# Performance work log

Measured on AMD Instinct MI355X. Metric: run time of the kernel, lower is better.

The kernel has to match this reference:

```python
import jax, jax.numpy as jnp
import numpy as np

NUM_GROUPS = 32
EPS = 1e-6


def group_norm(x, gamma, beta):
    # x: (B, C, H, W)
    B, C, H, W = x.shape
    g = x.reshape(B, NUM_GROUPS, C // NUM_GROUPS, H, W)
    mean = g.mean(axis=(2, 3, 4), keepdims=True)
    var = g.var(axis=(2, 3, 4), keepdims=True)
    g = (g - mean) / jnp.sqrt(var + EPS)
    g = g.reshape(B, C, H, W)
    return g * gamma[None, :, None, None] + beta[None, :, None, None]


def nin(x, W, b):
    # 1x1 linear projection over channel dim
    return jnp.einsum('bchw,cd->bdhw', x, W) + b[None, :, None, None]


def setup_inputs() -> dict:
    key = jax.random.key(0)
    ks = jax.random.split(key, 8)
    B, C, H, W = 32, 512, 32, 32
    lim = np.sqrt(3 * 0.1 / C)  # NIN init_scale=0.1 uniform limit
    return {
        'x': jax.random.normal(ks[0], (B, C, H, W), jnp.float32),
        'gamma': jnp.ones((C,), jnp.float32),
        'beta': jnp.zeros((C,), jnp.float32),
        'Wq': jax.random.uniform(ks[1], (C, C), jnp.float32, -lim, lim),
        'bq': jnp.zeros((C,), jnp.float32),
        'Wk': jax.random.uniform(ks[2], (C, C), jnp.float32, -lim, lim),
        'bk': jnp.zeros((C,), jnp.float32),
        'Wv': jax.random.uniform(ks[3], (C, C), jnp.float32, -lim, lim),
        'bv': jnp.zeros((C,), jnp.float32),
        'Wp': jax.random.normal(ks[4], (C, C), jnp.float32) * 1e-5,  # init_scale=0.0 -> ~0
        'bp': jnp.zeros((C,), jnp.float32),
    }


def reference(x, gamma, beta, Wq, bq, Wk, bk, Wv, bv, Wp, bp):
    B, C, H, W = x.shape
    h = group_norm(x, gamma, beta)
    q = nin(h, Wq, bq)
    k = nin(h, Wk, bk)
    v = nin(h, Wv, bv)
    # full (HW)x(HW) attention weights, as the original materializes
    w = jnp.einsum('bchw,bcHW->bhwHW', q, k) * (C ** -0.5)
    w = w.reshape(B, H, W, H * W)
    w = jax.nn.softmax(w, axis=-1)
    w = w.reshape(B, H, W, H, W)
    h_out = jnp.einsum('bhwHW,bcHW->bchw', w, v)
    h_out = nin(h_out, Wp, bp)
    return x + h_out
```

## Files before the change

kernel.cpp:

```cpp
#include <hip/hip_runtime.h>
#include <hip/hip_bf16.h>
#include <math.h>

typedef __attribute__((ext_vector_type(8))) short bf16x8;
typedef __attribute__((ext_vector_type(4))) float f32x4;

typedef const __attribute__((address_space(1))) unsigned int guint;
typedef __attribute__((address_space(3))) unsigned int luint;

static __device__ __forceinline__ short f2bf(float f) {
    union { float f; unsigned u; } a; a.f = f;
    unsigned r = 0x7FFFu + ((a.u >> 16) & 1u);
    return (short)((a.u + r) >> 16);
}
static __device__ __forceinline__ float bf2f(short s) {
    union { unsigned u; float f; } a;
    a.u = ((unsigned)(unsigned short)s) << 16;
    return a.f;
}

__global__ __launch_bounds__(256)
void cast_w3(const float* __restrict__ wq, const float* __restrict__ wk,
             const float* __restrict__ wv, short* __restrict__ out)
{
    const float* W = (blockIdx.y == 0) ? wq : (blockIdx.y == 1) ? wk : wv;
    short* O = out + (long long)blockIdx.y * 262144;
    int i = (blockIdx.x * 256 + threadIdx.x) * 8;
    float4 a = *reinterpret_cast<const float4*>(W + i);
    float4 b = *reinterpret_cast<const float4*>(W + i + 4);
    bf16x8 o;
    o[0] = f2bf(a.x); o[1] = f2bf(a.y); o[2] = f2bf(a.z); o[3] = f2bf(a.w);
    o[4] = f2bf(b.x); o[5] = f2bf(b.y); o[6] = f2bf(b.z); o[7] = f2bf(b.w);
    *reinterpret_cast<bf16x8*>(O + i) = o;
}

__global__ __launch_bounds__(256)
void transpose_w(const float* __restrict__ w0, const float* __restrict__ w1,
                 const float* __restrict__ w2, const float* __restrict__ w3,
                 short* __restrict__ outT, float qscale)
{
    __shared__ float ld[32][33];
    const float* W = (blockIdx.z == 0) ? w0 : (blockIdx.z == 1) ? w1
                   : (blockIdx.z == 2) ? w2 : w3;
    const float sc = (blockIdx.z == 0) ? qscale : 1.f;
    short* O = outT + (long long)blockIdx.z * 512 * 512;
    const int tx = threadIdx.x & 31, ty = threadIdx.x >> 5;
    const int c0 = blockIdx.y * 32, d0 = blockIdx.x * 32;
#pragma unroll
    for (int r = 0; r < 4; ++r)
        ld[ty + 8 * r][tx] = W[(long long)(c0 + ty + 8 * r) * 512 + d0 + tx];
    __syncthreads();
#pragma unroll
    for (int r = 0; r < 4; ++r)
        O[(long long)(d0 + ty + 8 * r) * 512 + c0 + tx] = f2bf(ld[tx][ty + 8 * r] * sc);
}

__global__ __launch_bounds__(256)
void vec_pre2(const float* __restrict__ Wp, const float* __restrict__ bp,
              const float* __restrict__ bv, const float* __restrict__ Wk,
              const float* __restrict__ bq, float* __restrict__ b2,
              float* __restrict__ wkbq)
{
    __shared__ float red[256];
    const int t = threadIdx.x;
    const int o = blockIdx.x * 32 + (t >> 3);
    const int part = t & 7;
    float a = 0.f;
    if (blockIdx.y == 0) {
        for (int d = part * 64; d < part * 64 + 64; ++d)
            a += bv[d] * Wp[d * 512 + o];
    } else {
        for (int d = part * 64; d < part * 64 + 64; ++d)
            a += Wk[o * 512 + d] * bq[d];
    }
    red[t] = a; __syncthreads();
    if (part < 4) red[t] += red[t + 4];
    __syncthreads();
    if (part < 2) red[t] += red[t + 2];
    __syncthreads();
    if (part == 0) {
        float v = red[t] + red[t + 1];
        if (blockIdx.y == 0) b2[o] = v + bp[o];
        else wkbq[o] = v;
    }
}

__global__ __launch_bounds__(256)
void small_nt(const short* __restrict__ A, const short* __restrict__ B,
              short* __restrict__ C, float scale, int K,
              int lda, int ldb, int ldc, int tilesM)
{
    __shared__ short lsA[128 * 64];
    __shared__ short lsB[128 * 64];
    const int m0 = (blockIdx.x % tilesM) * 128;
    const int n0 = (blockIdx.x / tilesM) * 128;
    const int t = threadIdx.x;
    const int lane = t & 63;
    const int w = t >> 6;
    const int wr = w >> 1, wc = w & 1;
    const int lr16 = lane & 15, lkg = lane >> 4;
    const int srow = 32 * w + (lane >> 3);
    const int scol = (lane & 7) * 8;
    const short* gA = A + (long long)(m0 + srow) * lda + scol;
    const short* gB = B + (long long)(n0 + srow) * ldb + scol;

    f32x4 acc[4][4];
#pragma unroll
    for (int i = 0; i < 4; ++i)
#pragma unroll
        for (int j = 0; j < 4; ++j) acc[i][j] = (f32x4){0.f, 0.f, 0.f, 0.f};

    const int nk = K >> 6;
    for (int kt = 0; kt < nk; ++kt) {
        const short* ga = gA + kt * 64;
        const short* gb = gB + kt * 64;
#pragma unroll
        for (int c = 0; c < 4; ++c) {
            __builtin_amdgcn_global_load_lds(
                (guint*)(ga + (long long)(8 * c) * lda),
                (luint*)&lsA[(32 * w + 8 * c) * 64], 16, 0, 0);
            __builtin_amdgcn_global_load_lds(
                (guint*)(gb + (long long)(8 * c) * ldb),
                (luint*)&lsB[(32 * w + 8 * c) * 64], 16, 0, 0);
        }
        __syncthreads();
#pragma unroll
        for (int ks = 0; ks < 2; ++ks) {
            bf16x8 af[4], bfr[4];
#pragma unroll
            for (int mi = 0; mi < 4; ++mi)
                af[mi] = *reinterpret_cast<const bf16x8*>(
                    &lsA[(wr * 64 + mi * 16 + lr16) * 64 + ks * 32 + lkg * 8]);
#pragma unroll
            for (int ni = 0; ni < 4; ++ni)
                bfr[ni] = *reinterpret_cast<const bf16x8*>(
                    &lsB[(wc * 64 + ni * 16 + lr16) * 64 + ks * 32 + lkg * 8]);
#pragma unroll
            for (int mi = 0; mi < 4; ++mi)
#pragma unroll
                for (int ni = 0; ni < 4; ++ni)
                    acc[mi][ni] = __builtin_amdgcn_mfma_f32_16x16x32_bf16(
                        af[mi], bfr[ni], acc[mi][ni], 0, 0, 0);
        }
        __syncthreads();
    }
#pragma unroll
    for (int mi = 0; mi < 4; ++mi)
#pragma unroll
        for (int ni = 0; ni < 4; ++ni) {
            const int col = n0 + wc * 64 + ni * 16 + lr16;
#pragma unroll
            for (int j = 0; j < 4; ++j) {
                const int rrow = m0 + wr * 64 + mi * 16 + lkg * 4 + j;
                C[(long long)rrow * ldc + col] = f2bf(acc[mi][ni][j] * scale);
            }
        }
}

__global__ __launch_bounds__(256)
void gn_fused(const float* __restrict__ x, const float* __restrict__ gamma,
              const float* __restrict__ beta, short* __restrict__ hn,
              short* __restrict__ hnT)
{
    __shared__ float xs[16 * 1024];
    __shared__ float red[256];
    const int bg = blockIdx.x;
    const int g  = bg & 31, b = bg >> 5;
    const int t  = threadIdx.x;
    const float4* px = reinterpret_cast<const float4*>(x + (long long)bg * 16384);
    float s = 0.f, ss = 0.f;
#pragma unroll
    for (int i = 0; i < 16; ++i) {
        float4 v = px[t + 256 * i];
        reinterpret_cast<float4*>(xs)[t + 256 * i] = v;
        s  += v.x + v.y + v.z + v.w;
        ss += v.x * v.x + v.y * v.y + v.z * v.z + v.w * v.w;
    }
    red[t] = s; __syncthreads();
    for (int o = 128; o > 0; o >>= 1) {
        if (t < o) red[t] += red[t + o];
        __syncthreads();
    }
    const float mean = red[0] * (1.f / 16384.f);
    __syncthreads();
    red[t] = ss; __syncthreads();
    for (int o = 128; o > 0; o >>= 1) {
        if (t < o) red[t] += red[t + o];
        __syncthreads();
    }
    const float var  = red[0] * (1.f / 16384.f) - mean * mean;
    const float rstd = rsqrtf(var + 1e-6f);

    const int half = t & 1;
    float ga[8], be[8];
#pragma unroll
    for (int cc = 0; cc < 8; ++cc) {
        ga[cc] = gamma[g * 16 + half * 8 + cc];
        be[cc] = beta[g * 16 + half * 8 + cc];
    }
    short* outB = hn + (long long)bg * 16384;
#pragma unroll
    for (int it = 0; it < 8; ++it) {
        const int sidx = it * 128 + (t >> 1);
        bf16x8 o;
#pragma unroll
        for (int cc = 0; cc < 8; ++cc) {
            float v = xs[(half * 8 + cc) * 1024 + sidx];
            o[cc] = f2bf((v - mean) * rstd * ga[cc] + be[cc]);
        }
        *reinterpret_cast<bf16x8*>(outB + sidx * 16 + half * 8) = o;
    }
    short* oT = hnT + ((long long)b * 512 + g * 16) * 1024;
#pragma unroll
    for (int cc = 0; cc < 16; ++cc) {
        const float g_ = gamma[g * 16 + cc], b_ = beta[g * 16 + cc];
        const int pos = t * 4;
        short4 o4;
        o4.x = f2bf((xs[cc * 1024 + pos + 0] - mean) * rstd * g_ + b_);
        o4.y = f2bf((xs[cc * 1024 + pos + 1] - mean) * rstd * g_ + b_);
        o4.z = f2bf((xs[cc * 1024 + pos + 2] - mean) * rstd * g_ + b_);
        o4.w = f2bf((xs[cc * 1024 + pos + 3] - mean) * rstd * g_ + b_);
        *reinterpret_cast<short4*>(oT + cc * 1024 + pos) = o4;
    }
}

__global__ __launch_bounds__(256)
void colv_k(const short* __restrict__ hnT, const float* __restrict__ wkbq,
            float* __restrict__ colv, float qs)
{
    const int b = blockIdx.y, j = blockIdx.x * 256 + threadIdx.x;
    const short* p = hnT + (long long)b * 512 * 1024 + j;
    float a = 0.f;
    for (int c = 0; c < 512; ++c) a += wkbq[c] * bf2f(p[c * 1024]);
    colv[b * 1024 + j] = a * qs;
}

template<int BIAS_M, int BIAS_NB, int RESID, int EXPRS, int DIVROW4, int HN_A, int HN_B>
__global__ __launch_bounds__(512, 1)
void nt_gemm(const short* __restrict__ A, const short* __restrict__ B,
             void* __restrict__ Cv,
             const float* __restrict__ biasM, const float* __restrict__ biasN,
             const float* __restrict__ resid, float* __restrict__ rs,
             float scale, int K, int lda, int ldb, int ldc,
             long long sA, long long sB, long long sC,
             int tilesM, int tilesPerBatch)
{
    __shared__ short lsA[2][2][128 * 64];
    __shared__ short lsB[2][2][128 * 64];

    const int id = blockIdx.x;
    const int chunk = gridDim.x >> 3;
    const int gid = chunk ? ((id & 7) * chunk + (id >> 3)) : id;
    const int bz = gid / tilesPerBatch;
    const int tt = gid - bz * tilesPerBatch;
    const int m0 = (tt % tilesM) * 256;
    const int n0 = (tt / tilesM) * 256;

    const int t = threadIdx.x;
    const int lane = t & 63;
    const int w = t >> 6;
    const int wrs = w >> 1;
    const int wcs = w & 1;
    const int lr16 = lane & 15, lkg = lane >> 4;
    const int sw = lr16 & 7;

    const int srow = t >> 3;
    const int jch  = (t & 7) ^ (srow & 7);
    const int scol = jch * 8;

    const short* gA; int rsA, ktA;
    if (HN_A) {
        gA = A + ((long long)bz * 32 + (jch >> 1)) * 16384
               + (long long)(m0 + srow) * 16 + (jch & 1) * 8;
        rsA = 16; ktA = 65536;
    } else {
        gA = A + (long long)bz * sA + (long long)(m0 + srow) * lda + scol;
        rsA = lda; ktA = 64;
    }
    const short* gB; int rsB, ktB;
    if (HN_B) {
        gB = B + ((long long)bz * 32 + (jch >> 1)) * 16384
               + (long long)(n0 + srow) * 16 + (jch & 1) * 8;
        rsB = 16; ktB = 65536;
    } else {
        gB = B + (long long)bz * sB + (long long)(n0 + srow) * ldb + scol;
        rsB = ldb; ktB = 64;
    }

    f32x4 acc[4][2][4];
#pragma unroll
    for (int q = 0; q < 4; ++q)
#pragma unroll
        for (int i = 0; i < 2; ++i)
#pragma unroll
            for (int j = 0; j < 4; ++j) acc[q][i][j] = (f32x4){0.f, 0.f, 0.f, 0.f};

    const int nk = K >> 6;

#define STAGE_A(buf, h, kt)                                                    \
    {                                                                          \
        _Pragma("unroll")                                                      \
        for (int c = 0; c < 2; ++c)                                            \
            __builtin_amdgcn_global_load_lds(                                  \
                (guint*)(gA + (long long)(kt) * ktA                            \
                            + (long long)((h) * 128 + 64 * c) * rsA),          \
                (luint*)&lsA[buf][h][t * 8 + 4096 * c], 16, 0, 0);             \
    }
#define STAGE_B(buf, h, kt)                                                    \
    {                                                                          \
        _Pragma("unroll")                                                      \
        for (int c = 0; c < 2; ++c)                                            \
            __builtin_amdgcn_global_load_lds(                                  \
                (guint*)(gB + (long long)(kt) * ktB                            \
                            + (long long)((h) * 128 + 64 * c) * rsB),          \
                (luint*)&lsB[buf][h][t * 8 + 4096 * c], 16, 0, 0);             \
    }

#define LDA_HALF(dst, buf, h)                                                  \
    _Pragma("unroll")                                                          \
    for (int mi2 = 0; mi2 < 2; ++mi2)                                          \
        _Pragma("unroll")                                                      \
        for (int ks = 0; ks < 2; ++ks)                                         \
            dst[mi2][ks] = *reinterpret_cast<const bf16x8*>(                   \
                &lsA[buf][h][(wrs * 32 + mi2 * 16 + lr16) * 64 +               \
                             (((ks * 4 + lkg) ^ sw) * 8)]);
#define LDB_HALF(dst, buf, h)                                                  \
    _Pragma("unroll")                                                          \
    for (int ni = 0; ni < 4; ++ni)                                             \
        _Pragma("unroll")                                                      \
        for (int ks = 0; ks < 2; ++ks)                                         \
            dst[ni][ks] = *reinterpret_cast<const bf16x8*>(                    \
                &lsB[buf][h][(wcs * 64 + ni * 16 + lr16) * 64 +                \
                             (((ks * 4 + lkg) ^ sw) * 8)]);

#define MFMAQ(q, Af, Bf)                                                       \
    _Pragma("unroll")                                                          \
    for (int ks = 0; ks < 2; ++ks)                                             \
        _Pragma("unroll")                                                      \
        for (int mi2 = 0; mi2 < 2; ++mi2)                                      \
            _Pragma("unroll")                                                  \
            for (int ni = 0; ni < 4; ++ni)                                     \
                acc[q][mi2][ni] = __builtin_amdgcn_mfma_f32_16x16x32_bf16(     \
                    Af[mi2][ks], Bf[ni][ks], acc[q][mi2][ni], 0, 0, 0);

#define PH_END(N)                                                              \
    asm volatile("s_waitcnt vmcnt(" #N ")" ::: "memory");                      \
    __builtin_amdgcn_s_barrier();                                              \
    __builtin_amdgcn_sched_barrier(0)

#define FRAME(b, kt)                                                           \
    {                                                                          \
        bf16x8 a0[2][2], a1[2][2], b0f[4][2], b1f[4][2];                       \
        LDB_HALF(b0f, b, 0)                                                    \
        LDA_HALF(a0, b, 0)                                                     \
        LDB_HALF(b1f, b, 1)                                                    \
        STAGE_B((b) ^ 1, 0, (kt) + 1);                                         \
        STAGE_B((b) ^ 1, 1, (kt) + 1);                                         \
        STAGE_A((b) ^ 1, 0, (kt) + 1);                                         \
        MFMAQ(0, a0, b0f)                                                      \
        MFMAQ(1, a0, b1f)                                                      \
        PH_END(6);                                                             \
        LDA_HALF(a1, b, 1)                                                     \
        STAGE_A((b) ^ 1, 1, (kt) + 1);                                         \
        MFMAQ(2, a1, b0f)                                                      \
        MFMAQ(3, a1, b1f)                                                      \
        PH_END(2);                                                             \
    }

    STAGE_B(0, 0, 0); STAGE_B(0, 1, 0); STAGE_A(0, 0, 0);
    STAGE_A(0, 1, 0);
    PH_END(2);

    for (int kt = 0; kt < nk; kt += 2) {
        FRAME(0, kt)
        FRAME(1, kt + 1)
    }
#undef STAGE_A
#undef STAGE_B
#undef LDA_HALF
#undef LDB_HALF
#undef MFMAQ
#undef PH_END
#undef FRAME

    float psum[2][2][4];
    if (EXPRS) {
#pragma unroll
        for (int ah = 0; ah < 2; ++ah)
#pragma unroll
            for (int mi2 = 0; mi2 < 2; ++mi2)
#pragma unroll
                for (int j = 0; j < 4; ++j) psum[ah][mi2][j] = 0.f;
    }
#pragma unroll
    for (int ah = 0; ah < 2; ++ah) {
#pragma unroll
        for (int bh = 0; bh < 2; ++bh) {
#pragma unroll
            for (int mi2 = 0; mi2 < 2; ++mi2) {
                float addm[4], mul[4];
#pragma unroll
                for (int j = 0; j < 4; ++j) {
                    const int rrow = m0 + ah * 128 + wrs * 32 + mi2 * 16 + lkg * 4 + j;
                    addm[j] = BIAS_M ? biasM[rrow] : 0.f;
                    if (DIVROW4) {
                        const float* r4 = rs + (long long)bz * 4096 + rrow;
                        mul[j] = 1.f / (r4[0] + r4[1024] + r4[2048] + r4[3072]);
                    } else mul[j] = 1.f;
                }
#pragma unroll
                for (int ni = 0; ni < 4; ++ni) {
                    const int col = n0 + bh * 128 + wcs * 64 + ni * 16 + lr16;
                    float bn = BIAS_NB ? biasN[(long long)bz * 1024 + col] : 0.f;
#pragma unroll
                    for (int j = 0; j < 4; ++j) {
                        const int rrow = m0 + ah * 128 + wrs * 32 + mi2 * 16 + lkg * 4 + j;
                        float v2 = acc[ah * 2 + bh][mi2][ni][j] + addm[j] + bn;
                        v2 *= scale;
                        if (EXPRS) { v2 = __expf(v2 - 8.f); psum[ah][mi2][j] += v2; }
                        if (DIVROW4) v2 *= mul[j];
                        const long long idx = (long long)rrow * ldc + col;
                        if (RESID) {
                            float* Cf = (float*)Cv + (long long)bz * sC;
                            Cf[idx] = v2 + resid[(long long)bz * sC + idx];
                        } else {
                            short* Cs = (short*)Cv + (long long)bz * sC;
                            Cs[idx] = f2bf(v2);
                        }
                    }
                }
            }
        }
    }
    if (EXPRS) {
#pragma unroll
        for (int ah = 0; ah < 2; ++ah)
#pragma unroll
            for (int mi2 = 0; mi2 < 2; ++mi2)
#pragma unroll
                for (int j = 0; j < 4; ++j) {
                    float v = psum[ah][mi2][j];
                    v += __shfl_xor(v, 1); v += __shfl_xor(v, 2);
                    v += __shfl_xor(v, 4); v += __shfl_xor(v, 8);
                    psum[ah][mi2][j] = v;
                }
        float* scr = (float*)&lsA[1][0][0];
        __syncthreads();
        if (lr16 == 0) {
#pragma unroll
            for (int ah = 0; ah < 2; ++ah)
#pragma unroll
                for (int mi2 = 0; mi2 < 2; ++mi2)
#pragma unroll
                    for (int j = 0; j < 4; ++j)
                        scr[wcs * 256 + ah * 128 + wrs * 32 + mi2 * 16 + lkg * 4 + j]
                            = psum[ah][mi2][j];
        }
        __syncthreads();
        if (t < 256)
            rs[(long long)bz * 4096 + (n0 >> 8) * 1024 + m0 + t]
                = scr[t] + scr[256 + t];
    }
}

extern "C" void kernel_launch(void* const* d_in, const int* in_sizes, int n_in,
                              void* d_out, int out_size, void* d_ws, size_t ws_size,
                              hipStream_t stream)
{
    (void)in_sizes; (void)n_in; (void)out_size; (void)ws_size;
    const float* x     = (const float*)d_in[0];
    const float* gamma = (const float*)d_in[1];
    const float* beta  = (const float*)d_in[2];
    const float* Wq = (const float*)d_in[3];
    const float* bq = (const float*)d_in[4];
    const float* Wk = (const float*)d_in[5];
    const float* bk = (const float*)d_in[6];  (void)bk;
    const float* Wv = (const float*)d_in[7];
    const float* bv = (const float*)d_in[8];
    const float* Wp = (const float*)d_in[9];
    const float* bp = (const float*)d_in[10];
    float* out = (float*)d_out;

    char* ws = (char*)d_ws;
    short*  wq_bf  = (short*)ws;
    short*  wk_bf  = wq_bf + 262144;
    short*  wv_bf  = wq_bf + 2 * 262144;
    short*  wpT_bf = wq_bf + 3 * 262144;
    short*  expS = (short*)ws;
    short*  hnT  = (short*)(ws + (64LL << 20));
    short*  tmp  = (short*)(ws + (96LL << 20));
    short*  hn   = (short*)(ws + (128LL << 20));
    short*  MqkT = (short*)(ws + (160LL << 20));
    short*  Avp  = MqkT + 262144;
    float*  rs4  = (float*)(ws + (161LL << 20));
    float*  colv = rs4 + 32 * 4096;
    float*  b2   = colv + 32 * 1024;
    float*  wkbq = b2 + 512;
    short*  Phn  = tmp;

    const float qscale = 0.044194173824159216f;

    cast_w3<<<dim3(128, 3), 256, 0, stream>>>(Wq, Wk, Wv, wq_bf);
    transpose_w<<<dim3(16, 16, 1), 256, 0, stream>>>(Wp, Wp, Wp, Wp, wpT_bf, 1.f);
    vec_pre2<<<dim3(16, 2), 256, 0, stream>>>(Wp, bp, bv, Wk, bq, b2, wkbq);
    small_nt<<<16, 256, 0, stream>>>(wk_bf, wq_bf, MqkT, qscale, 512, 512, 512, 512, 4);
    small_nt<<<16, 256, 0, stream>>>(wpT_bf, wv_bf, Avp, 1.f, 512, 512, 512, 512, 4);

    gn_fused<<<dim3(1024), 256, 0, stream>>>(x, gamma, beta, hn, hnT);
    colv_k<<<dim3(4, 32), 256, 0, stream>>>(hnT, wkbq, colv, qscale);

    nt_gemm<0, 0, 0, 0, 0, 1, 0><<<256, 512, 0, stream>>>(
        hn, MqkT, tmp, nullptr, nullptr, nullptr, nullptr, 1.f,
        512, 0, 512, 512, 0, 0, 512LL * 1024, 4, 8);
    nt_gemm<0, 1, 0, 1, 0, 0, 1><<<512, 512, 0, stream>>>(
        tmp, hn, expS, nullptr, colv, nullptr, rs4, 1.f,
        512, 512, 0, 1024, 512LL * 1024, 0, 1024LL * 1024, 4, 16);
    nt_gemm<0, 0, 0, 0, 1, 0, 0><<<256, 512, 0, stream>>>(
        expS, hnT, Phn, nullptr, nullptr, nullptr, rs4, 1.f,
        1024, 1024, 1024, 512, 1024LL * 1024, 512LL * 1024, 512LL * 1024, 4, 8);
    nt_gemm<1, 0, 1, 0, 0, 0, 0><<<256, 512, 0, stream>>>(
        Avp, Phn, out, b2, nullptr, x, nullptr, 1.f,
        512, 512, 512, 1024, 0, 512LL * 1024, 512LL * 1024, 2, 8);
}
```

Before: 226.8 us.

## Compute Q and K projections explicitly instead of folding Wk^T Wq into one matrix

Drops the precomputed Wk^T·Wq product and the colv bias correction kernel. Q and K are now produced together by one GEMM over hn with concatenated transposed weights and biases, and the score GEMM then multiplies Q by K directly. The row-sum scratch moves into the output buffer, and weight prep is merged into a single kernel. The projection GEMM gets twice the output width, but one small GEMM and the colv pass go away, and the score GEMM reads a [Q|K] buffer instead of hn.

```diff
diff --git a/kernel.cpp b/kernel.cpp
--- a/kernel.cpp
+++ b/kernel.cpp
@@ -20,32 +20,25 @@
 }
 
 __global__ __launch_bounds__(256)
-void cast_w3(const float* __restrict__ wq, const float* __restrict__ wk,
-             const float* __restrict__ wv, short* __restrict__ out)
-{
-    const float* W = (blockIdx.y == 0) ? wq : (blockIdx.y == 1) ? wk : wv;
-    short* O = out + (long long)blockIdx.y * 262144;
-    int i = (blockIdx.x * 256 + threadIdx.x) * 8;
-    float4 a = *reinterpret_cast<const float4*>(W + i);
-    float4 b = *reinterpret_cast<const float4*>(W + i + 4);
-    bf16x8 o;
-    o[0] = f2bf(a.x); o[1] = f2bf(a.y); o[2] = f2bf(a.z); o[3] = f2bf(a.w);
-    o[4] = f2bf(b.x); o[5] = f2bf(b.y); o[6] = f2bf(b.z); o[7] = f2bf(b.w);
-    *reinterpret_cast<bf16x8*>(O + i) = o;
-}
-
-__global__ __launch_bounds__(256)
-void transpose_w(const float* __restrict__ w0, const float* __restrict__ w1,
-                 const float* __restrict__ w2, const float* __restrict__ w3,
-                 short* __restrict__ outT, float qscale)
-{
-    __shared__ float ld[32][33];
-    const float* W = (blockIdx.z == 0) ? w0 : (blockIdx.z == 1) ? w1
-                   : (blockIdx.z == 2) ? w2 : w3;
-    const float sc = (blockIdx.z == 0) ? qscale : 1.f;
-    short* O = outT + (long long)blockIdx.z * 512 * 512;
+void prep_w(const float* __restrict__ Wq, const float* __restrict__ Wk,
+            const float* __restrict__ Wp, const float* __restrict__ Wv,
+            short* __restrict__ wT, float qscale)
+{
+    const int z = blockIdx.z;
     const int tx = threadIdx.x & 31, ty = threadIdx.x >> 5;
     const int c0 = blockIdx.y * 32, d0 = blockIdx.x * 32;
+    short* O = wT + (long long)z * 262144;
+    if (z == 3) {
+#pragma unroll
+        for (int r = 0; r < 4; ++r) {
+            const int idx = (c0 + ty + 8 * r) * 512 + d0 + tx;
+            O[idx] = f2bf(Wv[idx]);
+        }
+        return;
+    }
+    __shared__ float ld[32][33];
+    const float* W = (z == 0) ? Wq : (z == 1) ? Wk : Wp;
+    const float sc = (z == 0) ? qscale : 1.f;
 #pragma unroll
     for (int r = 0; r < 4; ++r)
         ld[ty + 8 * r][tx] = W[(long long)(c0 + ty + 8 * r) * 512 + d0 + tx];
@@ -56,33 +49,30 @@
 }
 
 __global__ __launch_bounds__(256)
-void vec_pre2(const float* __restrict__ Wp, const float* __restrict__ bp,
-              const float* __restrict__ bv, const float* __restrict__ Wk,
-              const float* __restrict__ bq, float* __restrict__ b2,
-              float* __restrict__ wkbq)
+void concat_bias(const float* __restrict__ bq, const float* __restrict__ bk,
+                 float* __restrict__ bqk, float qscale)
+{
+    int i = blockIdx.x * 256 + threadIdx.x;
+    bqk[i] = (i < 512) ? bq[i] * qscale : bk[i - 512];
+}
+
+__global__ __launch_bounds__(256)
+void b2_pre(const float* __restrict__ Wp, const float* __restrict__ bp,
+            const float* __restrict__ bv, float* __restrict__ b2)
 {
     __shared__ float red[256];
     const int t = threadIdx.x;
     const int o = blockIdx.x * 32 + (t >> 3);
     const int part = t & 7;
     float a = 0.f;
-    if (blockIdx.y == 0) {
-        for (int d = part * 64; d < part * 64 + 64; ++d)
-            a += bv[d] * Wp[d * 512 + o];
-    } else {
-        for (int d = part * 64; d < part * 64 + 64; ++d)
-            a += Wk[o * 512 + d] * bq[d];
-    }
+    for (int d = part * 64; d < part * 64 + 64; ++d)
+        a += bv[d] * Wp[d * 512 + o];
     red[t] = a; __syncthreads();
     if (part < 4) red[t] += red[t + 4];
     __syncthreads();
     if (part < 2) red[t] += red[t + 2];
     __syncthreads();
-    if (part == 0) {
-        float v = red[t] + red[t + 1];
-        if (blockIdx.y == 0) b2[o] = v + bp[o];
-        else wkbq[o] = v;
-    }
+    if (part == 0) b2[o] = red[t] + red[t + 1] + bp[o];
 }
 
 __global__ __launch_bounds__(256)
@@ -224,18 +214,7 @@
     }
 }
 
-__global__ __launch_bounds__(256)
-void colv_k(const short* __restrict__ hnT, const float* __restrict__ wkbq,
-            float* __restrict__ colv, float qs)
-{
-    const int b = blockIdx.y, j = blockIdx.x * 256 + threadIdx.x;
-    const short* p = hnT + (long long)b * 512 * 1024 + j;
-    float a = 0.f;
-    for (int c = 0; c < 512; ++c) a += wkbq[c] * bf2f(p[c * 1024]);
-    colv[b * 1024 + j] = a * qs;
-}
-
-template<int BIAS_M, int BIAS_NB, int RESID, int EXPRS, int DIVROW4, int HN_A, int HN_B>
+template<int BIAS_M, int BIAS_N, int RESID, int EXPRS, int DIVROW4, int HN_A, int HN_B>
 __global__ __launch_bounds__(512, 1)
 void nt_gemm(const short* __restrict__ A, const short* __restrict__ B,
              void* __restrict__ Cv,
@@ -411,7 +390,7 @@
 #pragma unroll
                 for (int ni = 0; ni < 4; ++ni) {
                     const int col = n0 + bh * 128 + wcs * 64 + ni * 16 + lr16;
-                    float bn = BIAS_NB ? biasN[(long long)bz * 1024 + col] : 0.f;
+                    float bn = BIAS_N ? biasN[col] : 0.f;
 #pragma unroll
                     for (int j = 0; j < 4; ++j) {
                         const int rrow = m0 + ah * 128 + wrs * 32 + mi2 * 16 + lkg * 4 + j;
@@ -474,7 +453,7 @@
     const float* Wq = (const float*)d_in[3];
     const float* bq = (const float*)d_in[4];
     const float* Wk = (const float*)d_in[5];
-    const float* bk = (const float*)d_in[6];  (void)bk;
+    const float* bk = (const float*)d_in[6];
     const float* Wv = (const float*)d_in[7];
     const float* bv = (const float*)d_in[8];
     const float* Wp = (const float*)d_in[9];
@@ -482,39 +461,36 @@
     float* out = (float*)d_out;
 
     char* ws = (char*)d_ws;
-    short*  wq_bf  = (short*)ws;
-    short*  wk_bf  = wq_bf + 262144;
-    short*  wv_bf  = wq_bf + 2 * 262144;
-    short*  wpT_bf = wq_bf + 3 * 262144;
-    short*  expS = (short*)ws;
-    short*  hnT  = (short*)(ws + (64LL << 20));
-    short*  tmp  = (short*)(ws + (96LL << 20));
-    short*  hn   = (short*)(ws + (128LL << 20));
-    short*  MqkT = (short*)(ws + (160LL << 20));
-    short*  Avp  = MqkT + 262144;
-    float*  rs4  = (float*)(ws + (161LL << 20));
-    float*  colv = rs4 + 32 * 4096;
-    float*  b2   = colv + 32 * 1024;
-    float*  wkbq = b2 + 512;
-    short*  Phn  = tmp;
+    short*  hnT  = (short*)ws;
+    short*  qkb  = (short*)(ws + (32LL << 20));
+    short*  hn   = (short*)(ws + (96LL << 20));
+    short*  expS = (short*)(ws + (96LL << 20));
+    short*  wT   = (short*)(ws + (160LL << 20));
+    short*  Avp  = (short*)(ws + (162LL << 20));
+    float*  bqk  = (float*)(ws + (162LL << 20) + (512 << 10));
+    float*  b2   = bqk + 1024;
+    short*  Phn  = qkb;
+    float*  rs4  = (float*)d_out;
+
+    const short* WqkT = wT;
+    const short* WpT  = wT + 2 * 262144;
+    const short* WvC  = wT + 3 * 262144;
 
     const float qscale = 0.044194173824159216f;
 
-    cast_w3<<<dim3(128, 3), 256, 0, stream>>>(Wq, Wk, Wv, wq_bf);
-    transpose_w<<<dim3(16, 16, 1), 256, 0, stream>>>(Wp, Wp, Wp, Wp, wpT_bf, 1.f);
-    vec_pre2<<<dim3(16, 2), 256, 0, stream>>>(Wp, bp, bv, Wk, bq, b2, wkbq);
-    small_nt<<<16, 256, 0, stream>>>(wk_bf, wq_bf, MqkT, qscale, 512, 512, 512, 512, 4);
-    small_nt<<<16, 256, 0, stream>>>(wpT_bf, wv_bf, Avp, 1.f, 512, 512, 512, 512, 4);
+    prep_w<<<dim3(16, 16, 4), 256, 0, stream>>>(Wq, Wk, Wp, Wv, wT, qscale);
+    concat_bias<<<dim3(4), 256, 0, stream>>>(bq, bk, bqk, qscale);
+    b2_pre<<<dim3(16), 256, 0, stream>>>(Wp, bp, bv, b2);
+    small_nt<<<16, 256, 0, stream>>>(WpT, WvC, Avp, 1.f, 512, 512, 512, 512, 4);
 
     gn_fused<<<dim3(1024), 256, 0, stream>>>(x, gamma, beta, hn, hnT);
-    colv_k<<<dim3(4, 32), 256, 0, stream>>>(hnT, wkbq, colv, qscale);
-
-    nt_gemm<0, 0, 0, 0, 0, 1, 0><<<256, 512, 0, stream>>>(
-        hn, MqkT, tmp, nullptr, nullptr, nullptr, nullptr, 1.f,
-        512, 0, 512, 512, 0, 0, 512LL * 1024, 4, 8);
-    nt_gemm<0, 1, 0, 1, 0, 0, 1><<<512, 512, 0, stream>>>(
-        tmp, hn, expS, nullptr, colv, nullptr, rs4, 1.f,
-        512, 512, 0, 1024, 512LL * 1024, 0, 1024LL * 1024, 4, 16);
+
+    nt_gemm<0, 1, 0, 0, 0, 1, 0><<<512, 512, 0, stream>>>(
+        hn, WqkT, qkb, nullptr, bqk, nullptr, nullptr, 1.f,
+        512, 0, 512, 1024, 0, 0, 1024LL * 1024, 4, 16);
+    nt_gemm<0, 0, 0, 1, 0, 0, 0><<<512, 512, 0, stream>>>(
+        qkb, qkb + 512, expS, nullptr, nullptr, nullptr, rs4, 1.f,
+        512, 1024, 1024, 1024, 1024LL * 1024, 1024LL * 1024, 1024LL * 1024, 4, 16);
     nt_gemm<0, 0, 0, 0, 1, 0, 0><<<256, 512, 0, stream>>>(
         expS, hnT, Phn, nullptr, nullptr, nullptr, rs4, 1.f,
         1024, 1024, 1024, 512, 1024LL * 1024, 512LL * 1024, 512LL * 1024, 4, 8);
```

Result: faster. 206.0 us (-9.2%).
